# Kernel tuning notes

Hardware: AMD Instinct MI355X
Metric: run time of the kernel (lower is better)

## Reference

```python
import jax, jax.numpy as jnp
import numpy as np

N_NODES = 100000
N_EDGES = 3200000
FEAT = 64  # pos(32) + vel(32)
OUT_DIM = 2


def setup_inputs() -> dict:
    key = jax.random.key(0)
    k1, k2, k3, k4, k5, k6, k7, k8 = jax.random.split(key, 8)
    pos = jax.random.normal(k1, (N_NODES, 32), dtype=jnp.float32)
    vel = jax.random.normal(k2, (N_NODES, 32), dtype=jnp.float32)
    edge_index = jax.random.randint(k3, (2, N_EDGES), 0, N_NODES, dtype=jnp.int64 if jax.config.jax_enable_x64 else jnp.int32)
    s = 1.0 / np.sqrt(FEAT)
    W_rel = jax.random.uniform(k4, (FEAT, FEAT), jnp.float32, -s, s)
    b_rel = jax.random.uniform(k5, (FEAT,), jnp.float32, -s, s)
    W_root = jax.random.uniform(k6, (FEAT, FEAT), jnp.float32, -s, s)
    W_pred = jax.random.uniform(k7, (FEAT, OUT_DIM), jnp.float32, -s, s)
    b_pred = jax.random.uniform(k8, (OUT_DIM,), jnp.float32, -s, s)
    return {"pos": pos, "vel": vel, "edge_index": edge_index,
            "W_rel": W_rel, "b_rel": b_rel, "W_root": W_root,
            "W_pred": W_pred, "b_pred": b_pred}


def reference(pos, vel, edge_index, W_rel, b_rel, W_root, W_pred, b_pred):
    # h = cat([pos, vel], -1)  -> [N, 64]
    h = jnp.concatenate([pos, vel], axis=-1)
    src, dst = edge_index[0], edge_index[1]
    # GraphConv (PyG, aggr='add'): out_i = lin_rel(sum_{j->i} h_j) + lin_root(h_i)
    msgs = h[src]  # [E, 64] irregular gather
    agg = jax.ops.segment_sum(msgs, dst, num_segments=N_NODES)  # [N, 64]
    conv_out = agg @ W_rel + b_rel + h @ W_root
    # lin_pred
    return conv_out @ W_pred + b_pred
```

## Files before the change

kernel.cpp:

```cpp
#include <hip/hip_runtime.h>

#define N_NODES 100000
#define N_EDGES 3200000
#define FEAT 64
#define OUT_DIM 2

#define SHIFT 8
#define S_NODES 256
#define K_BUCKETS 391
#define CAP 8704
#define NB 800
#define EPB (N_EDGES / NB)
#define SPLIT 8


__global__ void fold_weights_kernel(const float* __restrict__ W_rel,
                                    const float* __restrict__ b_rel,
                                    const float* __restrict__ W_root,
                                    const float* __restrict__ W_pred,
                                    const float* __restrict__ b_pred,
                                    float* __restrict__ M,
                                    int* __restrict__ gcount) {
    int t = threadIdx.x;
    if (t < 128) {
        int k = t >> 1, o = t & 1;
        float acc = 0.f;
        #pragma unroll
        for (int f = 0; f < FEAT; ++f) acc += W_rel[k * FEAT + f] * W_pred[f * OUT_DIM + o];
        M[t] = acc;
    } else {
        int tt = t - 128;
        int k = tt >> 1, o = tt & 1;
        float acc = 0.f;
        #pragma unroll
        for (int f = 0; f < FEAT; ++f) acc += W_root[k * FEAT + f] * W_pred[f * OUT_DIM + o];
        M[128 + tt] = acc;
    }
    if (t < OUT_DIM) {
        float acc = b_pred[t];
        #pragma unroll
        for (int f = 0; f < FEAT; ++f) acc += b_rel[f] * W_pred[f * OUT_DIM + t];
        M[256 + t] = acc;
    }
    for (int i = t; i < K_BUCKETS; i += 256) gcount[i] = 0;
}

__global__ __launch_bounds__(256) void node_kernel(const float* __restrict__ pos,
                                                   const float* __restrict__ vel,
                                                   const float* __restrict__ M,
                                                   float* __restrict__ y,
                                                   float* __restrict__ out) {
    __shared__ float sM[258];
    for (int i = threadIdx.x; i < 258; i += 256) sM[i] = M[i];
    __syncthreads();

    int n = blockIdx.x * 256 + threadIdx.x;
    if (n >= N_NODES) return;

    const float4* p4 = (const float4*)(pos + (size_t)n * 32);
    const float4* v4 = (const float4*)(vel + (size_t)n * 32);
    float h[FEAT];
    #pragma unroll
    for (int i = 0; i < 8; ++i) {
        float4 a = p4[i];
        h[i * 4 + 0] = a.x; h[i * 4 + 1] = a.y; h[i * 4 + 2] = a.z; h[i * 4 + 3] = a.w;
    }
    #pragma unroll
    for (int i = 0; i < 8; ++i) {
        float4 a = v4[i];
        h[32 + i * 4 + 0] = a.x; h[32 + i * 4 + 1] = a.y; h[32 + i * 4 + 2] = a.z; h[32 + i * 4 + 3] = a.w;
    }

    float rel0 = 0.f, rel1 = 0.f, ro0 = 0.f, ro1 = 0.f;
    #pragma unroll
    for (int k = 0; k < FEAT; ++k) {
        float hk = h[k];
        rel0 += hk * sM[2 * k + 0];
        rel1 += hk * sM[2 * k + 1];
        ro0  += hk * sM[128 + 2 * k + 0];
        ro1  += hk * sM[128 + 2 * k + 1];
    }
    ((float2*)y)[n]   = make_float2(rel0, rel1);
    ((float2*)out)[n] = make_float2(ro0 + sM[256], ro1 + sM[257]);
}

__global__ __launch_bounds__(256) void binscatter_kernel(const int* __restrict__ edges,
                                                         int* __restrict__ gcount,
                                                         unsigned* __restrict__ scat) {
    __shared__ int hist[K_BUCKETS];
    __shared__ int cur[K_BUCKETS];
    for (int i = threadIdx.x; i < K_BUCKETS; i += 256) hist[i] = 0;
    __syncthreads();

    const int4* d4 = (const int4*)(edges + N_EDGES) + blockIdx.x * (EPB / 4);
    for (int i = threadIdx.x; i < EPB / 4; i += 256) {
        int4 d = d4[i];
        atomicAdd(&hist[d.x >> SHIFT], 1);
        atomicAdd(&hist[d.y >> SHIFT], 1);
        atomicAdd(&hist[d.z >> SHIFT], 1);
        atomicAdd(&hist[d.w >> SHIFT], 1);
    }
    __syncthreads();

    for (int i = threadIdx.x; i < K_BUCKETS; i += 256)
        cur[i] = atomicAdd(&gcount[i], hist[i]);
    __syncthreads();

    const int4* s4 = (const int4*)(edges + blockIdx.x * EPB);
    for (int i = threadIdx.x; i < EPB / 4; i += 256) {
        int4 s = s4[i];
        int4 d = d4[i];
        int k, p;
        k = d.x >> SHIFT; p = atomicAdd(&cur[k], 1);
        if (p < CAP) scat[(size_t)k * CAP + p] = (unsigned)s.x | ((unsigned)(d.x & (S_NODES - 1)) << 17);
        k = d.y >> SHIFT; p = atomicAdd(&cur[k], 1);
        if (p < CAP) scat[(size_t)k * CAP + p] = (unsigned)s.y | ((unsigned)(d.y & (S_NODES - 1)) << 17);
        k = d.z >> SHIFT; p = atomicAdd(&cur[k], 1);
        if (p < CAP) scat[(size_t)k * CAP + p] = (unsigned)s.z | ((unsigned)(d.z & (S_NODES - 1)) << 17);
        k = d.w >> SHIFT; p = atomicAdd(&cur[k], 1);
        if (p < CAP) scat[(size_t)k * CAP + p] = (unsigned)s.w | ((unsigned)(d.w & (S_NODES - 1)) << 17);
    }
}

__global__ __launch_bounds__(256) void accum_kernel(const unsigned* __restrict__ scat,
                                                    const int* __restrict__ gcount,
                                                    const float* __restrict__ y,
                                                    float* __restrict__ out) {
    __shared__ float acc[S_NODES * 2];
    int t = threadIdx.x;
    acc[t] = 0.f;
    acc[t + S_NODES] = 0.f;
    __syncthreads();

    int k = blockIdx.x >> 3;
    int part = blockIdx.x & (SPLIT - 1);
    int c = gcount[k];
    if (c > CAP) c = CAP;
    int chunk = (c + SPLIT - 1) / SPLIT;
    int lo = part * chunk;
    int hi = lo + chunk;
    if (hi > c) hi = c;

    const unsigned* sl = scat + (size_t)k * CAP;
    const float2* y2 = (const float2*)y;
    for (int i = lo + t; i < hi; i += 256) {
        unsigned p = sl[i];
        int src = p & 0x1FFFF;
        int dl = p >> 17;
        float2 v = y2[src];
        atomicAdd(&acc[dl], v.x);
        atomicAdd(&acc[S_NODES + dl], v.y);
    }
    __syncthreads();

    int node = k * S_NODES + t;
    if (node < N_NODES) {
        float a0 = acc[t];
        float a1 = acc[t + S_NODES];
        if (a0 != 0.f) atomicAdd(&out[2 * (size_t)node + 0], a0);
        if (a1 != 0.f) atomicAdd(&out[2 * (size_t)node + 1], a1);
    }
}

extern "C" void kernel_launch(void* const* d_in, const int* in_sizes, int n_in,
                              void* d_out, int out_size, void* d_ws, size_t ws_size,
                              hipStream_t stream) {
    const float* pos    = (const float*)d_in[0];
    const float* vel    = (const float*)d_in[1];
    const int*   edges  = (const int*)d_in[2];
    const float* W_rel  = (const float*)d_in[3];
    const float* b_rel  = (const float*)d_in[4];
    const float* W_root = (const float*)d_in[5];
    const float* W_pred = (const float*)d_in[6];
    const float* b_pred = (const float*)d_in[7];
    float* out = (float*)d_out;

    char* ws = (char*)d_ws;
    float*    M      = (float*)ws;
    float*    y      = (float*)(ws + 2048);
    int*      gcount = (int*)(ws + 802048);
    unsigned* scat   = (unsigned*)(ws + 803712);

    fold_weights_kernel<<<1, 256, 0, stream>>>(W_rel, b_rel, W_root, W_pred, b_pred, M, gcount);

    int node_blocks = (N_NODES + 255) / 256;
    node_kernel<<<node_blocks, 256, 0, stream>>>(pos, vel, M, y, out);

    binscatter_kernel<<<NB, 256, 0, stream>>>(edges, gcount, scat);

    accum_kernel<<<K_BUCKETS * SPLIT, 256, 0, stream>>>(scat, gcount, y, out);
}
```

Baseline: 186.4 us.

## Replace bucketed scatter-accumulate with direct global atomics per edge

Removes the two-pass binning scheme (histogram, bucket scatter into workspace, then shared-memory accumulation per bucket) and replaces it with one kernel that gathers the projected 2-float source value per edge and atomically adds it into the destination output. This eliminates the intermediate scat buffer traffic and one kernel launch. In exchange it issues 6.4M global float atomics to random addresses, which may contend in L2. It also drops the CAP overflow truncation, so the result is correct for any degree distribution.

```diff
diff --git a/kernel.cpp b/kernel.cpp
--- a/kernel.cpp
+++ b/kernel.cpp
@@ -5,22 +5,13 @@
 #define FEAT 64
 #define OUT_DIM 2
 
-#define SHIFT 8
-#define S_NODES 256
-#define K_BUCKETS 391
-#define CAP 8704
-#define NB 800
-#define EPB (N_EDGES / NB)
-#define SPLIT 8
-
 
 __global__ void fold_weights_kernel(const float* __restrict__ W_rel,
                                     const float* __restrict__ b_rel,
                                     const float* __restrict__ W_root,
                                     const float* __restrict__ W_pred,
                                     const float* __restrict__ b_pred,
-                                    float* __restrict__ M,
-                                    int* __restrict__ gcount) {
+                                    float* __restrict__ M) {
     int t = threadIdx.x;
     if (t < 128) {
         int k = t >> 1, o = t & 1;
@@ -42,7 +33,6 @@
         for (int f = 0; f < FEAT; ++f) acc += b_rel[f] * W_pred[f * OUT_DIM + t];
         M[256 + t] = acc;
     }
-    for (int i = t; i < K_BUCKETS; i += 256) gcount[i] = 0;
 }
 
 __global__ __launch_bounds__(256) void node_kernel(const float* __restrict__ pos,
@@ -84,82 +74,31 @@
     ((float2*)out)[n] = make_float2(ro0 + sM[256], ro1 + sM[257]);
 }
 
-__global__ __launch_bounds__(256) void binscatter_kernel(const int* __restrict__ edges,
-                                                         int* __restrict__ gcount,
-                                                         unsigned* __restrict__ scat) {
-    __shared__ int hist[K_BUCKETS];
-    __shared__ int cur[K_BUCKETS];
-    for (int i = threadIdx.x; i < K_BUCKETS; i += 256) hist[i] = 0;
-    __syncthreads();
+__global__ __launch_bounds__(256) void edge_atomic_kernel(const int* __restrict__ edges,
+                                                          const float* __restrict__ y,
+                                                          float* __restrict__ out) {
+    int i = blockIdx.x * 256 + threadIdx.x;
+    if (i >= N_EDGES / 4) return;
 
-    const int4* d4 = (const int4*)(edges + N_EDGES) + blockIdx.x * (EPB / 4);
-    for (int i = threadIdx.x; i < EPB / 4; i += 256) {
-        int4 d = d4[i];
-        atomicAdd(&hist[d.x >> SHIFT], 1);
-        atomicAdd(&hist[d.y >> SHIFT], 1);
-        atomicAdd(&hist[d.z >> SHIFT], 1);
-        atomicAdd(&hist[d.w >> SHIFT], 1);
-    }
-    __syncthreads();
+    const int4* s4 = (const int4*)edges;
+    const int4* d4 = (const int4*)(edges + N_EDGES);
+    int4 s = s4[i];
+    int4 d = d4[i];
 
-    for (int i = threadIdx.x; i < K_BUCKETS; i += 256)
-        cur[i] = atomicAdd(&gcount[i], hist[i]);
-    __syncthreads();
+    const float2* y2 = (const float2*)y;
+    float2 v0 = y2[s.x];
+    float2 v1 = y2[s.y];
+    float2 v2 = y2[s.z];
+    float2 v3 = y2[s.w];
 
-    const int4* s4 = (const int4*)(edges + blockIdx.x * EPB);
-    for (int i = threadIdx.x; i < EPB / 4; i += 256) {
-        int4 s = s4[i];
-        int4 d = d4[i];
-        int k, p;
-        k = d.x >> SHIFT; p = atomicAdd(&cur[k], 1);
-        if (p < CAP) scat[(size_t)k * CAP + p] = (unsigned)s.x | ((unsigned)(d.x & (S_NODES - 1)) << 17);
-        k = d.y >> SHIFT; p = atomicAdd(&cur[k], 1);
-        if (p < CAP) scat[(size_t)k * CAP + p] = (unsigned)s.y | ((unsigned)(d.y & (S_NODES - 1)) << 17);
-        k = d.z >> SHIFT; p = atomicAdd(&cur[k], 1);
-        if (p < CAP) scat[(size_t)k * CAP + p] = (unsigned)s.z | ((unsigned)(d.z & (S_NODES - 1)) << 17);
-        k = d.w >> SHIFT; p = atomicAdd(&cur[k], 1);
-        if (p < CAP) scat[(size_t)k * CAP + p] = (unsigned)s.w | ((unsigned)(d.w & (S_NODES - 1)) << 17);
-    }
-}
-
-__global__ __launch_bounds__(256) void accum_kernel(const unsigned* __restrict__ scat,
-                                                    const int* __restrict__ gcount,
-                                                    const float* __restrict__ y,
-                                                    float* __restrict__ out) {
-    __shared__ float acc[S_NODES * 2];
-    int t = threadIdx.x;
-    acc[t] = 0.f;
-    acc[t + S_NODES] = 0.f;
-    __syncthreads();
-
-    int k = blockIdx.x >> 3;
-    int part = blockIdx.x & (SPLIT - 1);
-    int c = gcount[k];
-    if (c > CAP) c = CAP;
-    int chunk = (c + SPLIT - 1) / SPLIT;
-    int lo = part * chunk;
-    int hi = lo + chunk;
-    if (hi > c) hi = c;
-
-    const unsigned* sl = scat + (size_t)k * CAP;
-    const float2* y2 = (const float2*)y;
-    for (int i = lo + t; i < hi; i += 256) {
-        unsigned p = sl[i];
-        int src = p & 0x1FFFF;
-        int dl = p >> 17;
-        float2 v = y2[src];
-        atomicAdd(&acc[dl], v.x);
-        atomicAdd(&acc[S_NODES + dl], v.y);
-    }
-    __syncthreads();
-
-    int node = k * S_NODES + t;
-    if (node < N_NODES) {
-        float a0 = acc[t];
-        float a1 = acc[t + S_NODES];
-        if (a0 != 0.f) atomicAdd(&out[2 * (size_t)node + 0], a0);
-        if (a1 != 0.f) atomicAdd(&out[2 * (size_t)node + 1], a1);
-    }
+    atomicAdd(&out[2 * (size_t)d.x + 0], v0.x);
+    atomicAdd(&out[2 * (size_t)d.x + 1], v0.y);
+    atomicAdd(&out[2 * (size_t)d.y + 0], v1.x);
+    atomicAdd(&out[2 * (size_t)d.y + 1], v1.y);
+    atomicAdd(&out[2 * (size_t)d.z + 0], v2.x);
+    atomicAdd(&out[2 * (size_t)d.z + 1], v2.y);
+    atomicAdd(&out[2 * (size_t)d.w + 0], v3.x);
+    atomicAdd(&out[2 * (size_t)d.w + 1], v3.y);
 }
 
 extern "C" void kernel_launch(void* const* d_in, const int* in_sizes, int n_in,
@@ -176,17 +115,14 @@
     float* out = (float*)d_out;
 
     char* ws = (char*)d_ws;
-    float*    M      = (float*)ws;
-    float*    y      = (float*)(ws + 2048);
-    int*      gcount = (int*)(ws + 802048);
-    unsigned* scat   = (unsigned*)(ws + 803712);
+    float* M = (float*)ws;
+    float* y = (float*)(ws + 2048);
 
-    fold_weights_kernel<<<1, 256, 0, stream>>>(W_rel, b_rel, W_root, W_pred, b_pred, M, gcount);
+    fold_weights_kernel<<<1, 256, 0, stream>>>(W_rel, b_rel, W_root, W_pred, b_pred, M);
 
     int node_blocks = (N_NODES + 255) / 256;
     node_kernel<<<node_blocks, 256, 0, stream>>>(pos, vel, M, y, out);
 
-    binscatter_kernel<<<NB, 256, 0, stream>>>(edges, gcount, scat);
-
-    accum_kernel<<<K_BUCKETS * SPLIT, 256, 0, stream>>>(scat, gcount, y, out);
+    int edge_blocks = (N_EDGES / 4 + 255) / 256;
+    edge_atomic_kernel<<<edge_blocks, 256, 0, stream>>>(edges, y, out);
 }
```

New measurement: 417.6 us. 2.24x slower.
